# Kernel tuning notes

Measured on AMD Instinct MI355X. Metric: run time of the kernel, lower is better.

The kernel has to match this reference:

```python
import jax, jax.numpy as jnp
import numpy as np

IN_CH, OUT_CH = 64, 64
MODES1, MODES2 = 20, 20
B, H, W = 16, 256, 256


def setup_inputs() -> dict:
    key = jax.random.key(0)
    k_x, k1r, k1i, k2r, k2i = jax.random.split(key, 5)
    scale = 1.0 / (IN_CH * OUT_CH)
    wshape = (IN_CH, OUT_CH, MODES1, MODES2)
    return {
        "x": jax.random.normal(k_x, (B, IN_CH, H, W), dtype=jnp.float32),
        "w1r": scale * jax.random.uniform(k1r, wshape, dtype=jnp.float32),
        "w1i": scale * jax.random.uniform(k1i, wshape, dtype=jnp.float32),
        "w2r": scale * jax.random.uniform(k2r, wshape, dtype=jnp.float32),
        "w2i": scale * jax.random.uniform(k2i, wshape, dtype=jnp.float32),
    }


def reference(x, w1r, w1i, w2r, w2i):
    # x: [B, C_in, H, W] real
    b, _, size1, size2 = x.shape
    m1, m2 = w1r.shape[2], w1r.shape[3]
    out_ch = w1r.shape[1]

    x_ft = jnp.fft.rfft2(x)  # [B, C_in, H, W//2+1] complex
    w1 = (w1r + 1j * w1i).astype(jnp.complex64)
    w2 = (w2r + 1j * w2i).astype(jnp.complex64)

    # Complex spectral mixing on the retained low-frequency corners
    top = jnp.einsum("bixy,ioxy->boxy", x_ft[:, :, :m1, :m2], w1)
    bot = jnp.einsum("bixy,ioxy->boxy", x_ft[:, :, -m1:, :m2], w2)

    out_ft = jnp.zeros((b, out_ch, size1, size2 // 2 + 1), dtype=jnp.complex64)
    out_ft = out_ft.at[:, :, :m1, :m2].set(top)
    out_ft = out_ft.at[:, :, -m1:, :m2].set(bot)

    return jnp.fft.irfft2(out_ft, s=(size1, size2))  # [B, C_out, H, W]
```

## Files before the change

### kernel.cpp

```cpp
#include <hip/hip_runtime.h>
#include <cstddef>


constexpr float KTH = 6.28318530717958647692f / 256.0f;

__global__ __launch_bounds__(320) void dft_w_kernel(const float* __restrict__ x,
                                                    float2* __restrict__ X1) {
  __shared__ float xs[64 * 132];
  int tid = threadIdx.x;
  int slot = tid / 20;
  int kx   = tid % 20;
  size_t row0 = (size_t)blockIdx.x * 64;
  const float* xb = x + row0 * 256;

  float a0r = 0.f, a0i = 0.f, a1r = 0.f, a1i = 0.f;
  float a2r = 0.f, a2i = 0.f, a3r = 0.f, a3i = 0.f;
  float cr, srn;
  __sincosf((float)kx * KTH, &srn, &cr);
  srn = -srn;

  const float* base = xs + slot * 4 * 132;

  for (int chunk = 0; chunk < 2; ++chunk) {
    __syncthreads();
    for (int i = tid; i < 2048; i += 320) {
      int r  = i >> 5;
      int c4 = i & 31;
      float4 v = *(const float4*)(xb + (size_t)r * 256 + chunk * 128 + c4 * 4);
      *(float4*)(xs + r * 132 + c4 * 4) = v;
    }
    __syncthreads();

    for (int w0 = 0; w0 < 128; w0 += 16) {
      int wg = chunk * 128 + w0;
      int m = (kx * wg) & 255;
      float c, s;
      __sincosf((float)m * KTH, &s, &c);
      s = -s;
#pragma unroll
      for (int dw = 0; dw < 16; dw += 4) {
        float4 v0 = *(const float4*)(base + 0 * 132 + w0 + dw);
        float4 v1 = *(const float4*)(base + 1 * 132 + w0 + dw);
        float4 v2 = *(const float4*)(base + 2 * 132 + w0 + dw);
        float4 v3 = *(const float4*)(base + 3 * 132 + w0 + dw);
#define DFTW_STEP(e)                                                  \
        {                                                             \
          a0r = fmaf(v0.e, c, a0r); a0i = fmaf(v0.e, s, a0i);         \
          a1r = fmaf(v1.e, c, a1r); a1i = fmaf(v1.e, s, a1i);         \
          a2r = fmaf(v2.e, c, a2r); a2i = fmaf(v2.e, s, a2i);         \
          a3r = fmaf(v3.e, c, a3r); a3i = fmaf(v3.e, s, a3i);         \
          float cn = c * cr - s * srn;                                \
          s = fmaf(c, srn, s * cr);                                   \
          c = cn;                                                     \
        }
        DFTW_STEP(x) DFTW_STEP(y) DFTW_STEP(z) DFTW_STEP(w)
#undef DFTW_STEP
      }
    }
  }

  size_t ob = (row0 + (size_t)slot * 4) * 20 + (size_t)kx;
  X1[ob]      = make_float2(a0r, a0i);
  X1[ob + 20] = make_float2(a1r, a1i);
  X1[ob + 40] = make_float2(a2r, a2i);
  X1[ob + 60] = make_float2(a3r, a3i);
}

__global__ __launch_bounds__(448) void dft_h_kernel(const float2* __restrict__ X1,
                                                    float2* __restrict__ X2) {
  __shared__ float4 Xs4[256 * 10];
  int bc = blockIdx.x;
  const float4* src = (const float4*)(X1 + (size_t)bc * 5120);
  for (int i = threadIdx.x; i < 2560; i += 448) Xs4[i] = src[i];
  __syncthreads();

  int t = threadIdx.x;
  if (t < 400) {
    int ky_i = t / 10;
    int g    = t % 10;
    int ky = (ky_i < 20) ? ky_i : 216 + ky_i;
    float cr, srn;
    __sincosf((float)ky * KTH, &srn, &cr);
    srn = -srn;
    float ar0 = 0.f, ai0 = 0.f, ar1 = 0.f, ai1 = 0.f;
    for (int h0 = 0; h0 < 256; h0 += 16) {
      int m = (ky * h0) & 255;
      float c, s;
      __sincosf((float)m * KTH, &s, &c);
      s = -s;
#pragma unroll
      for (int dh = 0; dh < 16; ++dh) {
        float4 v = Xs4[(h0 + dh) * 10 + g];
        ar0 = fmaf(v.x, c, fmaf(-v.y, s, ar0));
        ai0 = fmaf(v.x, s, fmaf(v.y, c, ai0));
        ar1 = fmaf(v.z, c, fmaf(-v.w, s, ar1));
        ai1 = fmaf(v.z, s, fmaf(v.w, c, ai1));
        float cn = c * cr - s * srn;
        s = fmaf(c, srn, s * cr);
        c = cn;
      }
    }
    size_t ob = (size_t)bc * 800 + (size_t)ky_i * 20 + (size_t)g * 2;
    X2[ob]     = make_float2(ar0, ai0);
    X2[ob + 1] = make_float2(ar1, ai1);
  }
}

__global__ __launch_bounds__(256) void mix_kernel(const float2* __restrict__ X2,
                                                  const float* __restrict__ w1r,
                                                  const float* __restrict__ w1i,
                                                  const float* __restrict__ w2r,
                                                  const float* __restrict__ w2i,
                                                  float2* __restrict__ Z) {
  __shared__ float2 Xs[16 * 64];
  __shared__ float Wr[64 * 64];
  __shared__ float Wi[64 * 64];
  int blk = blockIdx.x;
  int j = blk / 20, kx = blk % 20;
  const float* wr; const float* wi; int moff;
  if (j < 20) { wr = w1r; wi = w1i; moff = j * 20 + kx; }
  else        { wr = w2r; wi = w2i; moff = (j - 20) * 20 + kx; }

  for (int io = threadIdx.x; io < 4096; io += 256) {
    Wr[io] = wr[(size_t)io * 400 + moff];
    Wi[io] = wi[(size_t)io * 400 + moff];
  }
  for (int bi = threadIdx.x; bi < 1024; bi += 256) {
    Xs[bi] = X2[(size_t)bi * 800 + blk];
  }
  __syncthreads();

  int b  = threadIdx.x >> 4;
  int o0 = (threadIdx.x & 15) * 4;
  float zr[4] = {0, 0, 0, 0}, zi[4] = {0, 0, 0, 0};
  for (int i = 0; i < 64; ++i) {
    float2 xv = Xs[b * 64 + i];
#pragma unroll
    for (int q = 0; q < 4; ++q) {
      float wrv = Wr[i * 64 + o0 + q];
      float wiv = Wi[i * 64 + o0 + q];
      zr[q] = fmaf(xv.x, wrv, fmaf(-xv.y, wiv, zr[q]));
      zi[q] = fmaf(xv.x, wiv, fmaf(xv.y, wrv, zi[q]));
    }
  }
#pragma unroll
  for (int q = 0; q < 4; ++q) {
    Z[(size_t)(b * 64 + o0 + q) * 800 + blk] = make_float2(zr[q], zi[q]);
  }
}

__global__ __launch_bounds__(256) void icd_kernel(const float2* __restrict__ Z,
                                                  float* __restrict__ out) {
  __shared__ float2 Zs[800];
  __shared__ float2 Ys[256 * 21];
  int bo = blockIdx.x;
  const float2* src = Z + (size_t)bo * 800;
  for (int i = threadIdx.x; i < 800; i += 256) Zs[i] = src[i];
  __syncthreads();

  {
    int h = threadIdx.x;
    float cr, sr;
    __sincosf((float)h * KTH, &sr, &cr);
    float accr[20], acci[20];
#pragma unroll
    for (int k = 0; k < 20; ++k) { accr[k] = 0.f; acci[k] = 0.f; }
    float c = 1.0f, s = 0.0f;
    for (int j = 0; j < 40; ++j) {
      if (j == 20) {
        int m = (236 * h) & 255;
        __sincosf((float)m * KTH, &s, &c);
      }
#pragma unroll
      for (int k = 0; k < 20; ++k) {
        float2 z = Zs[j * 20 + k];
        accr[k] = fmaf(z.x, c, fmaf(-z.y, s, accr[k]));
        acci[k] = fmaf(z.x, s, fmaf(z.y, c, acci[k]));
      }
      float cn = c * cr - s * sr;
      s = fmaf(c, sr, s * cr);
      c = cn;
    }
    float2* yrow = Ys + h * 21;
#pragma unroll
    for (int k = 0; k < 20; ++k) yrow[k] = make_float2(accr[k], acci[k]);
  }
  __syncthreads();

  int w = threadIdx.x;
  float cr, sr;
  __sincosf((float)w * KTH, &sr, &cr);
  float* outb = out + (size_t)bo * 65536;
  const float SC = 2.0f / 65536.0f;
  for (int h0 = 0; h0 < 256; h0 += 8) {
    float acc[8];
#pragma unroll
    for (int r = 0; r < 8; ++r) acc[r] = 0.5f * Ys[(h0 + r) * 21].x;
    float c = cr, s = sr;
#pragma unroll
    for (int k = 1; k < 20; ++k) {
#pragma unroll
      for (int r = 0; r < 8; ++r) {
        float2 y = Ys[(h0 + r) * 21 + k];
        acc[r] = fmaf(y.x, c, fmaf(-y.y, s, acc[r]));
      }
      float cn = c * cr - s * sr;
      s = fmaf(c, sr, s * cr);
      c = cn;
    }
#pragma unroll
    for (int r = 0; r < 8; ++r) {
      outb[(h0 + r) * 256 + w] = acc[r] * SC;
    }
  }
}

extern "C" void kernel_launch(void* const* d_in, const int* in_sizes, int n_in,
                              void* d_out, int out_size, void* d_ws, size_t ws_size,
                              hipStream_t stream) {
  const float* x   = (const float*)d_in[0];
  const float* w1r = (const float*)d_in[1];
  const float* w1i = (const float*)d_in[2];
  const float* w2r = (const float*)d_in[3];
  const float* w2i = (const float*)d_in[4];
  float* out = (float*)d_out;

  float2* X1  = (float2*)d_out;
  float2* wsc = (float2*)d_ws;
  float2* X2  = wsc;
  float2* Zb  = wsc + 819200;

  dft_w_kernel<<<4096, 320, 0, stream>>>(x, X1);
  dft_h_kernel<<<1024, 448, 0, stream>>>(X1, X2);
  mix_kernel  <<<800, 256, 0, stream>>>(X2, w1r, w1i, w2r, w2i, Zb);
  icd_kernel  <<<1024, 256, 0, stream>>>(Zb, out);
}
```

Baseline: 764.0 us.

## Exploit real-input symmetry in forward W-DFT and inverse W-synthesis

The forward W-direction DFT now folds each real row into even/odd parts (x[w]±x[256-w]) before multiplying, which halves the multiply-adds per output mode. Each thread now computes two modes for four rows, using a swizzled LDS layout, and blocks handle 128 rows. The final inverse step likewise computes the outputs at w and 256-w together from shared cosine and sine partial sums, with w=0 and w=128 handled separately. This cuts the trig-weighted FMA work in the two largest stages, in exchange for more complex indexing and fewer, larger blocks in dft_w.

```diff
diff --git a/kernel.cpp b/kernel.cpp
--- a/kernel.cpp
+++ b/kernel.cpp
@@ -6,64 +6,122 @@
 
 __global__ __launch_bounds__(320) void dft_w_kernel(const float* __restrict__ x,
                                                     float2* __restrict__ X1) {
-  __shared__ float xs[64 * 132];
-  int tid = threadIdx.x;
-  int slot = tid / 20;
-  int kx   = tid % 20;
-  size_t row0 = (size_t)blockIdx.x * 64;
+  __shared__ float uds[128 * 68];
+  __shared__ float xs0[128];
+  const int tid = threadIdx.x;
+  const int sl = tid / 10;
+  const int kp = tid - sl * 10;
+  const size_t row0 = (size_t)blockIdx.x * 128;
   const float* xb = x + row0 * 256;
 
-  float a0r = 0.f, a0i = 0.f, a1r = 0.f, a1i = 0.f;
-  float a2r = 0.f, a2i = 0.f, a3r = 0.f, a3i = 0.f;
-  float cr, srn;
-  __sincosf((float)kx * KTH, &srn, &cr);
-  srn = -srn;
-
-  const float* base = xs + slot * 4 * 132;
-
-  for (int chunk = 0; chunk < 2; ++chunk) {
+  float cr0, sr0, cr1, sr1;
+  __sincosf((float)(2 * kp) * KTH, &sr0, &cr0);
+  __sincosf((float)(2 * kp + 1) * KTH, &sr1, &cr1);
+
+  float re[4][2] = {};
+  float im[4][2] = {};
+
+  const int swc = sl & 3;
+  const float* ub = uds + sl * 4 * 68;
+
+  for (int c = 0; c < 4; ++c) {
     __syncthreads();
-    for (int i = tid; i < 2048; i += 320) {
-      int r  = i >> 5;
-      int c4 = i & 31;
-      float4 v = *(const float4*)(xb + (size_t)r * 256 + chunk * 128 + c4 * 4);
-      *(float4*)(xs + r * 132 + c4 * 4) = v;
+    if (tid < 256) {
+      const int row = tid >> 1;
+      const int hf = tid & 1;
+      const int base = c * 32 + hf * 16;
+      const float* xr = xb + (size_t)row * 256;
+      float4 fq0 = *(const float4*)(xr + base);
+      float4 fq1 = *(const float4*)(xr + base + 4);
+      float4 fq2 = *(const float4*)(xr + base + 8);
+      float4 fq3 = *(const float4*)(xr + base + 12);
+      float4 fq4 = *(const float4*)(xr + base + 16);
+      const float* xm = xr + (240 - base);
+      float4 mq0 = *(const float4*)(xm);
+      float4 mq1 = *(const float4*)(xm + 4);
+      float4 mq2 = *(const float4*)(xm + 8);
+      float4 mq3 = *(const float4*)(xm + 12);
+      if (c == 0 && hf == 0) xs0[row] = fq0.x;
+      float* urow = uds + row * 68;
+      const int sw = (row >> 2) & 3;
+#define STAGE_Q(q, fa, fb, m)                                         \
+      {                                                               \
+        float4 u, d;                                                  \
+        u.x = fa.y + m.w; d.x = fa.y - m.w;                           \
+        u.y = fa.z + m.z; d.y = fa.z - m.z;                           \
+        u.z = fa.w + m.y; d.z = fa.w - m.y;                           \
+        u.w = fb.x + m.x; d.w = fb.x - m.x;                           \
+        if (c == 3 && hf == 1 && (q) == 3) u.w *= 0.5f;    \
+        int col = (((hf * 4 + (q)) ^ sw) * 4);                        \
+        *(float4*)(urow + col) = u;                                   \
+        *(float4*)(urow + 32 + col) = d;                              \
+      }
+      STAGE_Q(0, fq0, fq1, mq3)
+      STAGE_Q(1, fq1, fq2, mq2)
+      STAGE_Q(2, fq2, fq3, mq1)
+      STAGE_Q(3, fq3, fq4, mq0)
+#undef STAGE_Q
     }
     __syncthreads();
 
-    for (int w0 = 0; w0 < 128; w0 += 16) {
-      int wg = chunk * 128 + w0;
-      int m = (kx * wg) & 255;
-      float c, s;
-      __sincosf((float)m * KTH, &s, &c);
-      s = -s;
-#pragma unroll
-      for (int dw = 0; dw < 16; dw += 4) {
-        float4 v0 = *(const float4*)(base + 0 * 132 + w0 + dw);
-        float4 v1 = *(const float4*)(base + 1 * 132 + w0 + dw);
-        float4 v2 = *(const float4*)(base + 2 * 132 + w0 + dw);
-        float4 v3 = *(const float4*)(base + 3 * 132 + w0 + dw);
-#define DFTW_STEP(e)                                                  \
+    for (int g = 0; g < 2; ++g) {
+      const int w1 = c * 32 + g * 16 + 1;
+      float c0, s0, c1, s1;
+      { int m = (2 * kp * w1) & 255;       __sincosf((float)m * KTH, &s0, &c0); }
+      { int m = ((2 * kp + 1) * w1) & 255; __sincosf((float)m * KTH, &s1, &c1); }
+#pragma unroll
+      for (int q = 0; q < 4; ++q) {
+        const int col = (((g * 4 + q) ^ swc) * 4);
+        float4 u0 = *(const float4*)(ub + col);
+        float4 d0 = *(const float4*)(ub + 32 + col);
+        float4 u1 = *(const float4*)(ub + 68 + col);
+        float4 d1 = *(const float4*)(ub + 68 + 32 + col);
+        float4 u2 = *(const float4*)(ub + 136 + col);
+        float4 d2 = *(const float4*)(ub + 136 + 32 + col);
+        float4 u3 = *(const float4*)(ub + 204 + col);
+        float4 d3 = *(const float4*)(ub + 204 + 32 + col);
+#define DSTEP(e)                                                      \
         {                                                             \
-          a0r = fmaf(v0.e, c, a0r); a0i = fmaf(v0.e, s, a0i);         \
-          a1r = fmaf(v1.e, c, a1r); a1i = fmaf(v1.e, s, a1i);         \
-          a2r = fmaf(v2.e, c, a2r); a2i = fmaf(v2.e, s, a2i);         \
-          a3r = fmaf(v3.e, c, a3r); a3i = fmaf(v3.e, s, a3i);         \
-          float cn = c * cr - s * srn;                                \
-          s = fmaf(c, srn, s * cr);                                   \
-          c = cn;                                                     \
+          re[0][0] = fmaf(u0.e, c0, re[0][0]);                        \
+          im[0][0] = fmaf(d0.e, s0, im[0][0]);                        \
+          re[1][0] = fmaf(u1.e, c0, re[1][0]);                        \
+          im[1][0] = fmaf(d1.e, s0, im[1][0]);                        \
+          re[2][0] = fmaf(u2.e, c0, re[2][0]);                        \
+          im[2][0] = fmaf(d2.e, s0, im[2][0]);                        \
+          re[3][0] = fmaf(u3.e, c0, re[3][0]);                        \
+          im[3][0] = fmaf(d3.e, s0, im[3][0]);                        \
+          re[0][1] = fmaf(u0.e, c1, re[0][1]);                        \
+          im[0][1] = fmaf(d0.e, s1, im[0][1]);                        \
+          re[1][1] = fmaf(u1.e, c1, re[1][1]);                        \
+          im[1][1] = fmaf(d1.e, s1, im[1][1]);                        \
+          re[2][1] = fmaf(u2.e, c1, re[2][1]);                        \
+          im[2][1] = fmaf(d2.e, s1, im[2][1]);                        \
+          re[3][1] = fmaf(u3.e, c1, re[3][1]);                        \
+          im[3][1] = fmaf(d3.e, s1, im[3][1]);                        \
+          float cn0 = c0 * cr0 - s0 * sr0;                            \
+          s0 = fmaf(c0, sr0, s0 * cr0);                               \
+          c0 = cn0;                                                   \
+          float cn1 = c1 * cr1 - s1 * sr1;                            \
+          s1 = fmaf(c1, sr1, s1 * cr1);                               \
+          c1 = cn1;                                                   \
         }
-        DFTW_STEP(x) DFTW_STEP(y) DFTW_STEP(z) DFTW_STEP(w)
-#undef DFTW_STEP
-      }
-    }
-  }
-
-  size_t ob = (row0 + (size_t)slot * 4) * 20 + (size_t)kx;
-  X1[ob]      = make_float2(a0r, a0i);
-  X1[ob + 20] = make_float2(a1r, a1i);
-  X1[ob + 40] = make_float2(a2r, a2i);
-  X1[ob + 60] = make_float2(a3r, a3i);
+        DSTEP(x) DSTEP(y) DSTEP(z) DSTEP(w)
+#undef DSTEP
+      }
+    }
+  }
+
+#pragma unroll
+  for (int r = 0; r < 4; ++r) {
+    float x0v = xs0[sl * 4 + r];
+    size_t ob = (row0 + (size_t)(sl * 4 + r)) * 20 + (size_t)(kp * 2);
+    float4 o;
+    o.x = re[r][0] + x0v;
+    o.y = -im[r][0];
+    o.z = re[r][1] + x0v;
+    o.w = -im[r][1];
+    *(float4*)(X1 + ob) = o;
+  }
 }
 
 __global__ __launch_bounds__(448) void dft_h_kernel(const float2* __restrict__ X1,
@@ -152,11 +210,14 @@
 __global__ __launch_bounds__(256) void icd_kernel(const float2* __restrict__ Z,
                                                   float* __restrict__ out) {
   __shared__ float2 Zs[800];
-  __shared__ float2 Ys[256 * 21];
+  __shared__ float4 Ys4[256 * 11];
   int bo = blockIdx.x;
   const float2* src = Z + (size_t)bo * 800;
   for (int i = threadIdx.x; i < 800; i += 256) Zs[i] = src[i];
   __syncthreads();
+
+  const float SC = 2.0f / 65536.0f;
+  float* outb = out + (size_t)bo * 65536;
 
   {
     int h = threadIdx.x;
@@ -181,36 +242,62 @@
       s = fmaf(c, sr, s * cr);
       c = cn;
     }
-    float2* yrow = Ys + h * 21;
-#pragma unroll
-    for (int k = 0; k < 20; ++k) yrow[k] = make_float2(accr[k], acci[k]);
+    float2* yrow = (float2*)(Ys4 + h * 11);
+    yrow[0] = make_float2(0.5f * accr[0], 0.5f * acci[0]);
+#pragma unroll
+    for (int k = 1; k < 20; ++k) yrow[k] = make_float2(accr[k], acci[k]);
+    float sum0 = 0.5f * accr[0];
+    float sum128 = 0.5f * accr[0];
+#pragma unroll
+    for (int k = 1; k < 20; ++k) {
+      sum0 += accr[k];
+      sum128 += (k & 1) ? -accr[k] : accr[k];
+    }
+    outb[h * 256] = sum0 * SC;
+    outb[h * 256 + 128] = sum128 * SC;
   }
   __syncthreads();
 
-  int w = threadIdx.x;
-  float cr, sr;
-  __sincosf((float)w * KTH, &sr, &cr);
-  float* outb = out + (size_t)bo * 65536;
-  const float SC = 2.0f / 65536.0f;
-  for (int h0 = 0; h0 < 256; h0 += 8) {
-    float acc[8];
-#pragma unroll
-    for (int r = 0; r < 8; ++r) acc[r] = 0.5f * Ys[(h0 + r) * 21].x;
-    float c = cr, s = sr;
-#pragma unroll
-    for (int k = 1; k < 20; ++k) {
-#pragma unroll
-      for (int r = 0; r < 8; ++r) {
-        float2 y = Ys[(h0 + r) * 21 + k];
-        acc[r] = fmaf(y.x, c, fmaf(-y.y, s, acc[r]));
-      }
-      float cn = c * cr - s * sr;
-      s = fmaf(c, sr, s * cr);
-      c = cn;
-    }
-#pragma unroll
-    for (int r = 0; r < 8; ++r) {
-      outb[(h0 + r) * 256 + w] = acc[r] * SC;
+  {
+    int t = threadIdx.x;
+    int hg = t >> 7;
+    int wt = t & 127;
+    if (wt != 0) {
+      float cw, sw;
+      __sincosf((float)wt * KTH, &sw, &cw);
+      float c2 = cw * cw - sw * sw;
+      float s2 = 2.0f * cw * sw;
+      int h0e = hg * 128;
+      for (int h0 = h0e; h0 < h0e + 128; h0 += 8) {
+        float P[8], Q[8];
+#pragma unroll
+        for (int r = 0; r < 8; ++r) { P[r] = 0.f; Q[r] = 0.f; }
+        float c0 = 1.0f, s0 = 0.0f;
+        float c1 = cw,   s1 = sw;
+        const float4* yb = Ys4 + h0 * 11;
+        for (int p = 0; p < 10; ++p) {
+#pragma unroll
+          for (int r = 0; r < 8; ++r) {
+            float4 y = yb[r * 11 + p];
+            P[r] = fmaf(y.x, c0, P[r]);
+            Q[r] = fmaf(y.y, s0, Q[r]);
+            P[r] = fmaf(y.z, c1, P[r]);
+            Q[r] = fmaf(y.w, s1, Q[r]);
+          }
+          float cn0 = c0 * c2 - s0 * s2;
+          s0 = fmaf(c0, s2, s0 * c2);
+          c0 = cn0;
+          float cn1 = c1 * c2 - s1 * s2;
+          s1 = fmaf(c1, s2, s1 * c2);
+          c1 = cn1;
+        }
+#pragma unroll
+        for (int r = 0; r < 8; ++r) {
+          float pv = P[r] * SC, qv = Q[r] * SC;
+          outb[(h0 + r) * 256 + wt] = pv - qv;
+          outb[(h0 + r) * 256 + 256 - wt] = pv + qv;
+        }
+      }
     }
   }
 }
@@ -230,7 +317,7 @@
   float2* X2  = wsc;
   float2* Zb  = wsc + 819200;
 
-  dft_w_kernel<<<4096, 320, 0, stream>>>(x, X1);
+  dft_w_kernel<<<2048, 320, 0, stream>>>(x, X1);
   dft_h_kernel<<<1024, 448, 0, stream>>>(X1, X2);
   mix_kernel  <<<800, 256, 0, stream>>>(X2, w1r, w1i, w2r, w2i, Zb);
   icd_kernel  <<<1024, 256, 0, stream>>>(Zb, out);
```

Measured after the change: 679.9 us. 1.12x faster.
